# Optimization experiments

Hardware: AMD Instinct MI355X
Metric: run time of the kernel (lower is better)

Reference implementation:

```python
import jax, jax.numpy as jnp
import numpy as np

B, N, NB, P = 4, 2048, 10, 5
BIG = 1.0e5  # fill value for non-positive gt grasps


def _build_grasps(approach, base, contacts, thickness):
    # approach/base/contacts: [B,N,3], thickness: [B,N] -> [B,N,4,4]
    cross = jnp.cross(approach, base)
    R = jnp.stack([base, cross, approach], axis=-1)            # columns: [base, cross, approach]
    t = contacts + thickness[..., None] * 0.5 * base           # [B,N,3]
    top = jnp.concatenate([R, t[..., None]], axis=-1)          # [B,N,3,4]
    bottom = jnp.broadcast_to(jnp.array([0.0, 0.0, 0.0, 1.0], top.dtype),
                              top.shape[:-2] + (1, 4))
    return jnp.concatenate([top, bottom], axis=-2)             # [B,N,4,4]


def _transform_cps(cp_h, grasps):
    # cp_h: [P,4], grasps: [B,N,4,4] -> transformed control points [B,N,P,3]
    # torch: matmul(control_points, grasps^T)[..., :3]
    return jnp.einsum('pk,bnjk->bnpj', cp_h, grasps)[..., :3]


def _pairwise_sq(a, b):
    # a: [B,Na,P,3], b: [B,Nb,P,3] -> [B,Na,Nb] = sum_{p,c} (a-b)^2
    af = a.reshape(a.shape[0], a.shape[1], -1)
    bf = b.reshape(b.shape[0], b.shape[1], -1)
    a2 = jnp.sum(af * af, axis=-1)
    b2 = jnp.sum(bf * bf, axis=-1)
    d = a2[:, :, None] + b2[:, None, :] - 2.0 * jnp.einsum('bnd,bmd->bnm', af, bf)
    return jnp.maximum(d, 0.0)


def _forward(grasp_dir_head, approach_dir_head, grasp_offset_head, pred_points,
             binary_score_pred, binary_score_head, dir_labels_pc_cam, offset_labels_pc,
             grasp_success_labels_pc, approach_labels_pc_cam, bin_vals, bin_weights,
             control_pts, sym_control_pts):
    succ = grasp_success_labels_pc                              # [B,N] in {0,1}
    pos_in_view = jnp.maximum(jnp.sum(succ, axis=1), 1.0)       # min_geom_loss_divisor = 1.0

    # bin_offsets=True: lookup bin value of argmax bin
    thickness_pred = bin_vals[jnp.argmax(grasp_offset_head, axis=2)]   # [B,N]
    thickness_gt = bin_vals[jnp.argmax(offset_labels_pc, axis=2)]      # [B,N]

    pred_grasps = _build_grasps(approach_dir_head, grasp_dir_head, pred_points, thickness_pred)
    gt_grasps = _build_grasps(approach_labels_pc_cam, dir_labels_pc_cam, pred_points, thickness_gt)
    mask4 = succ.astype(bool)[:, :, None, None]
    pos_gt_grasps = jnp.where(mask4, gt_grasps, jnp.full_like(gt_grasps, BIG))

    ones_col = jnp.ones((P, 1), dtype=control_pts.dtype)
    cp_h = jnp.concatenate([control_pts, ones_col], axis=1)      # [P,4]
    scp_h = jnp.concatenate([sym_control_pts, ones_col], axis=1)

    pred_cp = _transform_cps(cp_h, pred_grasps)                  # [B,N,P,3]
    gt_cp_pos = _transform_cps(cp_h, pos_gt_grasps)
    sym_gt_cp_pos = _transform_cps(scp_h, pos_gt_grasps)

    # pred -> gt ADD-S (top-k with k=1 == min over concat of the two [B,N,N])
    d1 = _pairwise_sq(pred_cp, gt_cp_pos)
    d2 = _pairwise_sq(pred_cp, sym_gt_cp_pos)
    best = jnp.min(jnp.minimum(d1, d2), axis=2)                  # [B,N]
    gate = jnp.minimum(jnp.sum(succ, axis=1, keepdims=True), 1.0)
    min_adds = gate * jnp.sqrt(best)
    adds_loss = jnp.mean(binary_score_pred[:, :, 0] * min_adds)

    # gt -> pred ADD-S with unmasked gt grasps + confidence gather
    gt_cp = _transform_cps(cp_h, gt_grasps)
    sym_gt_cp = _transform_cps(scp_h, gt_grasps)
    dg1 = _pairwise_sq(gt_cp, pred_cp)                           # [B,Ngt,Npred]
    dg2 = _pairwise_sq(sym_gt_cp, pred_cp)
    m1 = jnp.min(dg1, axis=2); i1 = jnp.argmin(dg1, axis=2)
    m2 = jnp.min(dg2, axis=2); i2 = jnp.argmin(dg2, axis=2)
    # torch: where(-m1 < -m2, sym_idcs, idcs) == pick sym when m2 < m1
    idcs = jnp.where(m2 < m1, i2, i1)                            # [B,N]
    min_g2p = jnp.minimum(m1, m2) * succ
    conf = jnp.take_along_axis(binary_score_pred[:, :, 0], idcs, axis=1)
    adds_loss_gt2pred = jnp.mean(jnp.sum(conf * min_g2p, axis=1) / pos_in_view)

    # direction cosine loss
    cos_d = 1.0 - jnp.sum(dir_labels_pc_cam * grasp_dir_head, axis=2)
    dir_cosine_loss = jnp.mean(jnp.sum(cos_d * succ, axis=1) / pos_in_view)

    # approach cosine loss against orthogonalized label
    proj = jnp.sum(grasp_dir_head * approach_labels_pc_cam, axis=2, keepdims=True)
    orthog = approach_labels_pc_cam - proj * grasp_dir_head
    orthog = orthog / jnp.maximum(jnp.linalg.norm(orthog, axis=2, keepdims=True), 1e-12)
    cos_a = 1.0 - jnp.sum(orthog * approach_dir_head, axis=2)
    approach_cosine_loss = jnp.mean(jnp.sum(cos_a * succ, axis=1) / pos_in_view)

    # per-bin sigmoid BCE offset loss, bin-weighted
    bce = (offset_labels_pc * jax.nn.softplus(-grasp_offset_head)
           + (1.0 - offset_labels_pc) * jax.nn.softplus(grasp_offset_head))
    off = jnp.mean(bin_weights[None, None, :] * bce, axis=2)
    offset_loss = jnp.mean(jnp.sum(off * succ, axis=1) / pos_in_view)

    # binary success score BCE
    s = succ[:, :, None]
    score_bce = (s * jax.nn.softplus(-binary_score_head)
                 + (1.0 - s) * jax.nn.softplus(binary_score_head))
    bin_ce_loss = jnp.mean(score_bce)

    total = (1.0 * dir_cosine_loss + 1.0 * bin_ce_loss + 1.0 * offset_loss
             + 1.0 * approach_cosine_loss + 10.0 * adds_loss + 1.0 * adds_loss_gt2pred)
    return total


def setup_inputs():
    key = jax.random.key(0)
    ks = jax.random.split(key, 14)
    unit = lambda x: x / jnp.linalg.norm(x, axis=-1, keepdims=True)
    grasp_dir_head = unit(jax.random.normal(ks[0], (B, N, 3), jnp.float32))
    approach_dir_head = unit(jax.random.normal(ks[1], (B, N, 3), jnp.float32))
    grasp_offset_head = jax.random.normal(ks[2], (B, N, NB), jnp.float32)
    pred_points = jax.random.normal(ks[3], (B, N, 3), jnp.float32) * 0.3
    binary_score_pred = jax.random.uniform(ks[4], (B, N, 1), jnp.float32)
    binary_score_head = jax.random.normal(ks[5], (B, N, 1), jnp.float32)
    dir_labels_pc_cam = unit(jax.random.normal(ks[6], (B, N, 3), jnp.float32))
    offset_labels_pc = jax.nn.one_hot(jax.random.randint(ks[7], (B, N), 0, NB), NB, dtype=jnp.float32)
    grasp_success_labels_pc = jnp.round(jax.random.uniform(ks[8], (B, N), jnp.float32))
    approach_labels_pc_cam = unit(jax.random.normal(ks[9], (B, N, 3), jnp.float32))
    bin_vals = jnp.sort(jax.random.uniform(ks[10], (NB,), jnp.float32) * 0.075)
    bin_weights = jax.random.uniform(ks[11], (NB,), jnp.float32) + 0.5
    control_pts = jax.random.normal(ks[12], (P, 3), jnp.float32) * 0.05
    sym_control_pts = control_pts[jnp.array([0, 1, 3, 2, 4])]  # finger-swapped (symmetric) gripper
    return {
        'grasp_dir_head': grasp_dir_head,
        'approach_dir_head': approach_dir_head,
        'grasp_offset_head': grasp_offset_head,
        'pred_points': pred_points,
        'binary_score_pred': binary_score_pred,
        'binary_score_head': binary_score_head,
        'dir_labels_pc_cam': dir_labels_pc_cam,
        'offset_labels_pc': offset_labels_pc,
        'grasp_success_labels_pc': grasp_success_labels_pc,
        'approach_labels_pc_cam': approach_labels_pc_cam,
        'bin_vals': bin_vals,
        'bin_weights': bin_weights,
        'control_pts': control_pts,
        'sym_control_pts': sym_control_pts,
    }


def reference(grasp_dir_head, approach_dir_head, grasp_offset_head, pred_points,
              binary_score_pred, binary_score_head, dir_labels_pc_cam, offset_labels_pc,
              grasp_success_labels_pc, approach_labels_pc_cam, bin_vals, bin_weights,
              control_pts, sym_control_pts):
    return _forward(grasp_dir_head, approach_dir_head, grasp_offset_head, pred_points,
                    binary_score_pred, binary_score_head, dir_labels_pc_cam, offset_labels_pc,
                    grasp_success_labels_pc, approach_labels_pc_cam, bin_vals, bin_weights,
                    control_pts, sym_control_pts)
```

## Files before the change

### kernel.cpp

```cpp
#include <hip/hip_runtime.h>

#define Bn 4
#define Nn 2048
#define NBn 10
#define BN (Bn*Nn)
#define TM 64

#define OFF_PRED 0
#define OFF_GT   (BN*16)
#define OFF_SYM  (2*BN*16)
#define OFF_PN2  (3*BN*16)
#define OFF_GN2  (OFF_PN2 + BN)
#define OFF_SN2  (OFF_GN2 + BN)
#define OFF_BEST (OFF_SN2 + BN)
#define OFF_PK1  (OFF_BEST + BN)
#define OFF_PK2  (OFF_PK1 + 2*BN)
#define OFF_PART (OFF_PK2 + 2*BN)

__device__ inline float sp_(float x) {
  return fmaxf(x, 0.0f) + log1pf(expf(-fabsf(x)));
}

__device__ inline float dot16_(const float4&a0,const float4&a1,const float4&a2,const float4&a3,
                               const float4&b0,const float4&b1,const float4&b2,const float4&b3){
  float s0 = fmaf(a0.w,b0.w, fmaf(a0.z,b0.z, fmaf(a0.y,b0.y, a0.x*b0.x)));
  float s1 = fmaf(a1.w,b1.w, fmaf(a1.z,b1.z, fmaf(a1.y,b1.y, a1.x*b1.x)));
  float s2 = fmaf(a2.w,b2.w, fmaf(a2.z,b2.z, fmaf(a2.y,b2.y, a2.x*b2.x)));
  float s3 = fmaf(a3.w,b3.w, fmaf(a3.z,b3.z, fmaf(a3.y,b3.y, a3.x*b3.x)));
  return (s0+s1)+(s2+s3);
}

__device__ inline float blockSum_(float v, float* red) {
  #pragma unroll
  for (int o = 32; o > 0; o >>= 1) v += __shfl_down(v, o, 64);
  __syncthreads();
  if ((threadIdx.x & 63) == 0) red[threadIdx.x >> 6] = v;
  __syncthreads();
  return red[0] + red[1] + red[2] + red[3];
}

__global__ __launch_bounds__(64) void k_prep(
    const float* __restrict__ gdir, const float* __restrict__ adirp,
    const float* __restrict__ goff, const float* __restrict__ ppts,
    const float* __restrict__ dlab, const float* __restrict__ olab,
    const float* __restrict__ alab,
    const float* __restrict__ binv,
    const float* __restrict__ cpts, const float* __restrict__ scpts,
    float* __restrict__ ws)
{
  const int idx = blockIdx.x * 64 + threadIdx.x;

  const float gd0=gdir[idx*3+0],  gd1=gdir[idx*3+1],  gd2=gdir[idx*3+2];
  const float ad0=adirp[idx*3+0], ad1=adirp[idx*3+1], ad2=adirp[idx*3+2];
  const float dl0=dlab[idx*3+0],  dl1=dlab[idx*3+1],  dl2=dlab[idx*3+2];
  const float al0=alab[idx*3+0],  al1=alab[idx*3+1],  al2=alab[idx*3+2];
  const float pt0=ppts[idx*3+0],  pt1=ppts[idx*3+1],  pt2=ppts[idx*3+2];

  float bv = goff[idx*NBn]; int ap = 0;
  #pragma unroll
  for (int k = 1; k < NBn; k++) { float v = goff[idx*NBn+k]; if (v > bv) { bv = v; ap = k; } }
  float bg = olab[idx*NBn]; int ag = 0;
  #pragma unroll
  for (int k = 1; k < NBn; k++) { float v = olab[idx*NBn+k]; if (v > bg) { bg = v; ag = k; } }
  const float tp = binv[ap] * 0.5f;
  const float tg = binv[ag] * 0.5f;

  const float cp0 = ad1*gd2 - ad2*gd1, cp1 = ad2*gd0 - ad0*gd2, cp2 = ad0*gd1 - ad1*gd0;
  const float cg0 = al1*dl2 - al2*dl1, cg1 = al2*dl0 - al0*dl2, cg2 = al0*dl1 - al1*dl0;
  const float tpx = pt0 + tp*gd0, tpy = pt1 + tp*gd1, tpz = pt2 + tp*gd2;
  const float tgx = pt0 + tg*dl0, tgy = pt1 + tg*dl1, tgz = pt2 + tg*dl2;

  float pcp[15], gcp[15], hcp[15];
  float pn2 = 0.f, gn2 = 0.f, sn2 = 0.f;
  #pragma unroll
  for (int p = 0; p < 5; p++) {
    const float cx = cpts[p*3], cy = cpts[p*3+1], cz = cpts[p*3+2];
    const float sx = scpts[p*3], sy = scpts[p*3+1], sz = scpts[p*3+2];
    float x, y, z;
    x = gd0*cx + cp0*cy + ad0*cz + tpx;
    y = gd1*cx + cp1*cy + ad1*cz + tpy;
    z = gd2*cx + cp2*cy + ad2*cz + tpz;
    pcp[p*3+0]=x; pcp[p*3+1]=y; pcp[p*3+2]=z;
    pn2 = fmaf(x,x, fmaf(y,y, fmaf(z,z, pn2)));
    x = dl0*cx + cg0*cy + al0*cz + tgx;
    y = dl1*cx + cg1*cy + al1*cz + tgy;
    z = dl2*cx + cg2*cy + al2*cz + tgz;
    gcp[p*3+0]=x; gcp[p*3+1]=y; gcp[p*3+2]=z;
    gn2 = fmaf(x,x, fmaf(y,y, fmaf(z,z, gn2)));
    x = dl0*sx + cg0*sy + al0*sz + tgx;
    y = dl1*sx + cg1*sy + al1*sz + tgy;
    z = dl2*sx + cg2*sy + al2*sz + tgz;
    hcp[p*3+0]=x; hcp[p*3+1]=y; hcp[p*3+2]=z;
    sn2 = fmaf(x,x, fmaf(y,y, fmaf(z,z, sn2)));
  }

  float4* pd = (float4*)(ws + OFF_PRED) + (size_t)idx*4;
  pd[0]=make_float4(pcp[0],pcp[1],pcp[2],pcp[3]);
  pd[1]=make_float4(pcp[4],pcp[5],pcp[6],pcp[7]);
  pd[2]=make_float4(pcp[8],pcp[9],pcp[10],pcp[11]);
  pd[3]=make_float4(pcp[12],pcp[13],pcp[14],0.f);
  float4* gdst = (float4*)(ws + OFF_GT) + (size_t)idx*4;
  gdst[0]=make_float4(gcp[0],gcp[1],gcp[2],gcp[3]);
  gdst[1]=make_float4(gcp[4],gcp[5],gcp[6],gcp[7]);
  gdst[2]=make_float4(gcp[8],gcp[9],gcp[10],gcp[11]);
  gdst[3]=make_float4(gcp[12],gcp[13],gcp[14],0.f);
  float4* sdst = (float4*)(ws + OFF_SYM) + (size_t)idx*4;
  sdst[0]=make_float4(hcp[0],hcp[1],hcp[2],hcp[3]);
  sdst[1]=make_float4(hcp[4],hcp[5],hcp[6],hcp[7]);
  sdst[2]=make_float4(hcp[8],hcp[9],hcp[10],hcp[11]);
  sdst[3]=make_float4(hcp[12],hcp[13],hcp[14],0.f);
  ws[OFF_PN2+idx] = pn2; ws[OFF_GN2+idx] = gn2; ws[OFF_SN2+idx] = sn2;

  ((unsigned*)ws)[OFF_BEST + idx] = 0x7F800000u;
  ((unsigned long long*)(ws + OFF_PK1))[idx] = ~0ull;
  ((unsigned long long*)(ws + OFF_PK2))[idx] = ~0ull;
}

__global__ __launch_bounds__(256) void k_pair(const float* __restrict__ succ,
                                              float* __restrict__ ws) {
  __shared__ float4 gts[TM][4], sys[TM][4], prs[TM][4];
  __shared__ float gb2[TM], sb2[TM], pb2[TM], msk[TM];
  const int mt = blockIdx.x, nt = blockIdx.y, b = blockIdx.z;
  const int tid = threadIdx.x;
  const int r = tid >> 2, p = tid & 3;
  const int mrow = b*Nn + mt*TM + r;
  gts[r][p] = ((const float4*)(ws + OFF_GT))  [(size_t)mrow*4 + p];
  sys[r][p] = ((const float4*)(ws + OFF_SYM)) [(size_t)mrow*4 + p];
  prs[r][p] = ((const float4*)(ws + OFF_PRED))[(size_t)mrow*4 + p];
  if      (p == 0) gb2[r] = ws[OFF_GN2 + mrow];
  else if (p == 1) sb2[r] = ws[OFF_SN2 + mrow];
  else if (p == 2) pb2[r] = ws[OFF_PN2 + mrow];
  else             msk[r] = succ[mrow];
  __syncthreads();

  const int nrow = b*Nn + nt*256 + tid;
  const float INF = __int_as_float(0x7F800000);

  {
    const float4* pa = (const float4*)(ws + OFF_PRED) + (size_t)nrow*4;
    const float4 a0 = pa[0], a1 = pa[1], a2 = pa[2], a3 = pa[3];
    const float an2 = ws[OFF_PN2 + nrow];
    float best = INF;
    for (int m = 0; m < TM; m++) {
      if (msk[m] != 0.0f) {
        const float d1 = fmaxf(fmaf(-2.f, dot16_(a0,a1,a2,a3, gts[m][0],gts[m][1],gts[m][2],gts[m][3]), an2 + gb2[m]), 0.f);
        const float d2 = fmaxf(fmaf(-2.f, dot16_(a0,a1,a2,a3, sys[m][0],sys[m][1],sys[m][2],sys[m][3]), an2 + sb2[m]), 0.f);
        best = fminf(best, fminf(d1, d2));
      }
    }
    if (best < INF)
      atomicMin((unsigned int*)ws + OFF_BEST + nrow, __float_as_uint(best));
  }

  {
    const float4* g = (const float4*)(ws + OFF_GT)  + (size_t)nrow*4;
    const float4 g0=g[0], g1=g[1], g2=g[2], g3=g[3];
    const float4* s = (const float4*)(ws + OFF_SYM) + (size_t)nrow*4;
    const float4 s0=s[0], s1=s[1], s2=s[2], s3=s[3];
    const float gn2 = ws[OFF_GN2 + nrow], sn2 = ws[OFF_SN2 + nrow];
    unsigned long long b1 = ~0ull, b2 = ~0ull;
    for (int m = 0; m < TM; m++) {
      const float4 p0 = prs[m][0], p1 = prs[m][1], p2 = prs[m][2], p3 = prs[m][3];
      const float pb = pb2[m];
      const float d1 = fmaxf(fmaf(-2.f, dot16_(g0,g1,g2,g3,p0,p1,p2,p3), gn2 + pb), 0.f);
      const float d2 = fmaxf(fmaf(-2.f, dot16_(s0,s1,s2,s3,p0,p1,p2,p3), sn2 + pb), 0.f);
      const unsigned long long c1 = ((unsigned long long)__float_as_uint(d1) << 32) | (unsigned)(mt*TM + m);
      const unsigned long long c2 = ((unsigned long long)__float_as_uint(d2) << 32) | (unsigned)(mt*TM + m);
      b1 = (c1 < b1) ? c1 : b1;
      b2 = (c2 < b2) ? c2 : b2;
    }
    atomicMin((unsigned long long*)(ws + OFF_PK1) + nrow, b1);
    atomicMin((unsigned long long*)(ws + OFF_PK2) + nrow, b2);
  }
}

__global__ __launch_bounds__(256) void k_red(
    const float* __restrict__ bsp,  const float* __restrict__ bsh,
    const float* __restrict__ succ,
    const float* __restrict__ gdir, const float* __restrict__ adirp,
    const float* __restrict__ dlab, const float* __restrict__ alab,
    const float* __restrict__ goff, const float* __restrict__ olab,
    const float* __restrict__ binw,
    float* __restrict__ ws)
{
  __shared__ float red[4];
  const int b = blockIdx.y, nt = blockIdx.x;
  const int idx = b*Nn + nt*256 + threadIdx.x;
  const float sc = succ[idx];

  const float best = __uint_as_float(((const unsigned*)ws)[OFF_BEST + idx]);
  const float adds = (best < 1e30f) ? bsp[idx] * sqrtf(best) : 0.f;

  const unsigned long long p1 = ((const unsigned long long*)(ws + OFF_PK1))[idx];
  const unsigned long long p2 = ((const unsigned long long*)(ws + OFF_PK2))[idx];
  const float m1 = __uint_as_float((unsigned)(p1 >> 32));
  const float m2 = __uint_as_float((unsigned)(p2 >> 32));
  const int   i1 = (int)(p1 & 0xffffffffull);
  const int   i2 = (int)(p2 & 0xffffffffull);
  const int   id = (m2 < m1) ? i2 : i1;
  const float g2p = bsp[b*Nn + id] * fminf(m1, m2) * sc;

  const float gd0=gdir[idx*3+0],  gd1=gdir[idx*3+1],  gd2=gdir[idx*3+2];
  const float ad0=adirp[idx*3+0], ad1=adirp[idx*3+1], ad2=adirp[idx*3+2];
  const float dl0=dlab[idx*3+0],  dl1=dlab[idx*3+1],  dl2=dlab[idx*3+2];
  const float al0=alab[idx*3+0],  al1=alab[idx*3+1],  al2=alab[idx*3+2];

  const float cosd = 1.f - (dl0*gd0 + dl1*gd1 + dl2*gd2);
  const float proj = gd0*al0 + gd1*al1 + gd2*al2;
  const float o0 = al0 - proj*gd0, o1 = al1 - proj*gd1, o2 = al2 - proj*gd2;
  const float on = sqrtf(o0*o0 + o1*o1 + o2*o2);
  const float inv = 1.f / fmaxf(on, 1e-12f);
  const float cosa = 1.f - inv*(o0*ad0 + o1*ad1 + o2*ad2);

  float offv = 0.f;
  #pragma unroll
  for (int k = 0; k < NBn; k++) {
    const float x = goff[idx*NBn+k], lab = olab[idx*NBn+k];
    const float bce = lab * sp_(-x) + (1.f - lab) * sp_(x);
    offv = fmaf(binw[k], bce, offv);
  }
  offv *= (1.0f / NBn);
  const float sb = bsh[idx];
  const float sbce = sc * sp_(-sb) + (1.f - sc) * sp_(sb);

  float* part = ws + OFF_PART + (size_t)(b*8 + nt)*8;
  float t;
  t = blockSum_(cosd*sc, red); if (threadIdx.x == 0) part[0] = t;
  t = blockSum_(cosa*sc, red); if (threadIdx.x == 0) part[1] = t;
  t = blockSum_(offv*sc, red); if (threadIdx.x == 0) part[2] = t;
  t = blockSum_(sc, red);      if (threadIdx.x == 0) part[3] = t;
  t = blockSum_(sbce, red);    if (threadIdx.x == 0) part[4] = t;
  t = blockSum_(adds, red);    if (threadIdx.x == 0) part[5] = t;
  t = blockSum_(g2p, red);     if (threadIdx.x == 0) part[6] = t;
}

__global__ __launch_bounds__(64) void k_fin(const float* __restrict__ ws, float* __restrict__ out) {
  const int t = threadIdx.x;
  float v[7];
  #pragma unroll
  for (int c = 0; c < 7; c++) v[c] = (t < 32) ? ws[OFF_PART + t*8 + c] : 0.f;
  #pragma unroll
  for (int o = 1; o < 8; o <<= 1) {
    #pragma unroll
    for (int c = 0; c < 7; c++) v[c] += __shfl_xor(v[c], o, 64);
  }
  const float pos = fmaxf(v[3], 1.f);
  float vb   = (v[0] + v[1] + v[2] + v[6]) / pos;
  float bce  = v[4];
  float adds = v[5];
  #pragma unroll
  for (int o = 8; o < 32; o <<= 1) {
    vb   += __shfl_xor(vb,   o, 64);
    bce  += __shfl_xor(bce,  o, 64);
    adds += __shfl_xor(adds, o, 64);
  }
  if (t == 0)
    out[0] = vb * 0.25f + bce * (1.f/BN) + 10.f * adds * (1.f/BN);
}

extern "C" void kernel_launch(void* const* d_in, const int* in_sizes, int n_in,
                              void* d_out, int out_size, void* d_ws, size_t ws_size,
                              hipStream_t stream) {
  const float* gdir  = (const float*)d_in[0];
  const float* adirp = (const float*)d_in[1];
  const float* goff  = (const float*)d_in[2];
  const float* ppts  = (const float*)d_in[3];
  const float* bsp   = (const float*)d_in[4];
  const float* bsh   = (const float*)d_in[5];
  const float* dlab  = (const float*)d_in[6];
  const float* olab  = (const float*)d_in[7];
  const float* succ  = (const float*)d_in[8];
  const float* alab  = (const float*)d_in[9];
  const float* binv  = (const float*)d_in[10];
  const float* binw  = (const float*)d_in[11];
  const float* cpts  = (const float*)d_in[12];
  const float* scpts = (const float*)d_in[13];
  float* ws  = (float*)d_ws;
  float* out = (float*)d_out;

  k_prep<<<dim3(BN/64), dim3(64), 0, stream>>>(gdir, adirp, goff, ppts,
                                               dlab, olab, alab, binv, cpts, scpts, ws);
  k_pair<<<dim3(Nn/TM, Nn/256, Bn), dim3(256), 0, stream>>>(succ, ws);
  k_red<<<dim3(Nn/256, Bn), dim3(256), 0, stream>>>(bsp, bsh, succ, gdir, adirp,
                                                    dlab, alab, goff, olab, binw, ws);
  k_fin<<<1, 64, 0, stream>>>(ws, out);
}
```

Before: 136.4 us.

## Fuse per-point losses into prep, register-block pair kernel, merge tail reductions

Moves the per-point direction, approach, offset and score BCE losses into the prep kernel, so one fewer kernel launch is needed and the inputs are read once. The pairwise kernel now gives each thread two query rows with a smaller M tile, replaces the success-mask branch with a large additive bias, and tracks the argmin in plain float/int before packing a single combined 64-bit atomic. The separate reduce and final kernels become one 1024-thread tail kernel. In exchange, the pair kernel uses more registers, the tail runs on a single block, and it relies on __threadfence_block rather than a barrier between the LDS writes and reads by other lanes.

```diff
diff --git a/kernel.cpp b/kernel.cpp
--- a/kernel.cpp
+++ b/kernel.cpp
@@ -4,7 +4,8 @@
 #define Nn 2048
 #define NBn 10
 #define BN (Bn*Nn)
-#define TM 64
+#define TM 32
+#define BIGM 1e32f
 
 #define OFF_PRED 0
 #define OFF_GT   (BN*16)
@@ -13,9 +14,8 @@
 #define OFF_GN2  (OFF_PN2 + BN)
 #define OFF_SN2  (OFF_GN2 + BN)
 #define OFF_BEST (OFF_SN2 + BN)
-#define OFF_PK1  (OFF_BEST + BN)
-#define OFF_PK2  (OFF_PK1 + 2*BN)
-#define OFF_PART (OFF_PK2 + 2*BN)
+#define OFF_PK   (OFF_BEST + BN)
+#define OFF_PART (OFF_PK + 2*BN)
 
 __device__ inline float sp_(float x) {
   return fmaxf(x, 0.0f) + log1pf(expf(-fabsf(x)));
@@ -39,22 +39,26 @@
   return red[0] + red[1] + red[2] + red[3];
 }
 
-__global__ __launch_bounds__(64) void k_prep(
+__global__ __launch_bounds__(256) void k_prep(
     const float* __restrict__ gdir, const float* __restrict__ adirp,
     const float* __restrict__ goff, const float* __restrict__ ppts,
+    const float* __restrict__ bsh,
     const float* __restrict__ dlab, const float* __restrict__ olab,
-    const float* __restrict__ alab,
-    const float* __restrict__ binv,
+    const float* __restrict__ succ, const float* __restrict__ alab,
+    const float* __restrict__ binv, const float* __restrict__ binw,
     const float* __restrict__ cpts, const float* __restrict__ scpts,
     float* __restrict__ ws)
 {
-  const int idx = blockIdx.x * 64 + threadIdx.x;
+  __shared__ float red[4];
+  const int pb = blockIdx.x;
+  const int idx = pb * 256 + threadIdx.x;
 
   const float gd0=gdir[idx*3+0],  gd1=gdir[idx*3+1],  gd2=gdir[idx*3+2];
   const float ad0=adirp[idx*3+0], ad1=adirp[idx*3+1], ad2=adirp[idx*3+2];
   const float dl0=dlab[idx*3+0],  dl1=dlab[idx*3+1],  dl2=dlab[idx*3+2];
   const float al0=alab[idx*3+0],  al1=alab[idx*3+1],  al2=alab[idx*3+2];
   const float pt0=ppts[idx*3+0],  pt1=ppts[idx*3+1],  pt2=ppts[idx*3+2];
+  const float sc = succ[idx];
 
   float bv = goff[idx*NBn]; int ap = 0;
   #pragma unroll
@@ -112,98 +116,7 @@
   ws[OFF_PN2+idx] = pn2; ws[OFF_GN2+idx] = gn2; ws[OFF_SN2+idx] = sn2;
 
   ((unsigned*)ws)[OFF_BEST + idx] = 0x7F800000u;
-  ((unsigned long long*)(ws + OFF_PK1))[idx] = ~0ull;
-  ((unsigned long long*)(ws + OFF_PK2))[idx] = ~0ull;
-}
-
-__global__ __launch_bounds__(256) void k_pair(const float* __restrict__ succ,
-                                              float* __restrict__ ws) {
-  __shared__ float4 gts[TM][4], sys[TM][4], prs[TM][4];
-  __shared__ float gb2[TM], sb2[TM], pb2[TM], msk[TM];
-  const int mt = blockIdx.x, nt = blockIdx.y, b = blockIdx.z;
-  const int tid = threadIdx.x;
-  const int r = tid >> 2, p = tid & 3;
-  const int mrow = b*Nn + mt*TM + r;
-  gts[r][p] = ((const float4*)(ws + OFF_GT))  [(size_t)mrow*4 + p];
-  sys[r][p] = ((const float4*)(ws + OFF_SYM)) [(size_t)mrow*4 + p];
-  prs[r][p] = ((const float4*)(ws + OFF_PRED))[(size_t)mrow*4 + p];
-  if      (p == 0) gb2[r] = ws[OFF_GN2 + mrow];
-  else if (p == 1) sb2[r] = ws[OFF_SN2 + mrow];
-  else if (p == 2) pb2[r] = ws[OFF_PN2 + mrow];
-  else             msk[r] = succ[mrow];
-  __syncthreads();
-
-  const int nrow = b*Nn + nt*256 + tid;
-  const float INF = __int_as_float(0x7F800000);
-
-  {
-    const float4* pa = (const float4*)(ws + OFF_PRED) + (size_t)nrow*4;
-    const float4 a0 = pa[0], a1 = pa[1], a2 = pa[2], a3 = pa[3];
-    const float an2 = ws[OFF_PN2 + nrow];
-    float best = INF;
-    for (int m = 0; m < TM; m++) {
-      if (msk[m] != 0.0f) {
-        const float d1 = fmaxf(fmaf(-2.f, dot16_(a0,a1,a2,a3, gts[m][0],gts[m][1],gts[m][2],gts[m][3]), an2 + gb2[m]), 0.f);
-        const float d2 = fmaxf(fmaf(-2.f, dot16_(a0,a1,a2,a3, sys[m][0],sys[m][1],sys[m][2],sys[m][3]), an2 + sb2[m]), 0.f);
-        best = fminf(best, fminf(d1, d2));
-      }
-    }
-    if (best < INF)
-      atomicMin((unsigned int*)ws + OFF_BEST + nrow, __float_as_uint(best));
-  }
-
-  {
-    const float4* g = (const float4*)(ws + OFF_GT)  + (size_t)nrow*4;
-    const float4 g0=g[0], g1=g[1], g2=g[2], g3=g[3];
-    const float4* s = (const float4*)(ws + OFF_SYM) + (size_t)nrow*4;
-    const float4 s0=s[0], s1=s[1], s2=s[2], s3=s[3];
-    const float gn2 = ws[OFF_GN2 + nrow], sn2 = ws[OFF_SN2 + nrow];
-    unsigned long long b1 = ~0ull, b2 = ~0ull;
-    for (int m = 0; m < TM; m++) {
-      const float4 p0 = prs[m][0], p1 = prs[m][1], p2 = prs[m][2], p3 = prs[m][3];
-      const float pb = pb2[m];
-      const float d1 = fmaxf(fmaf(-2.f, dot16_(g0,g1,g2,g3,p0,p1,p2,p3), gn2 + pb), 0.f);
-      const float d2 = fmaxf(fmaf(-2.f, dot16_(s0,s1,s2,s3,p0,p1,p2,p3), sn2 + pb), 0.f);
-      const unsigned long long c1 = ((unsigned long long)__float_as_uint(d1) << 32) | (unsigned)(mt*TM + m);
-      const unsigned long long c2 = ((unsigned long long)__float_as_uint(d2) << 32) | (unsigned)(mt*TM + m);
-      b1 = (c1 < b1) ? c1 : b1;
-      b2 = (c2 < b2) ? c2 : b2;
-    }
-    atomicMin((unsigned long long*)(ws + OFF_PK1) + nrow, b1);
-    atomicMin((unsigned long long*)(ws + OFF_PK2) + nrow, b2);
-  }
-}
-
-__global__ __launch_bounds__(256) void k_red(
-    const float* __restrict__ bsp,  const float* __restrict__ bsh,
-    const float* __restrict__ succ,
-    const float* __restrict__ gdir, const float* __restrict__ adirp,
-    const float* __restrict__ dlab, const float* __restrict__ alab,
-    const float* __restrict__ goff, const float* __restrict__ olab,
-    const float* __restrict__ binw,
-    float* __restrict__ ws)
-{
-  __shared__ float red[4];
-  const int b = blockIdx.y, nt = blockIdx.x;
-  const int idx = b*Nn + nt*256 + threadIdx.x;
-  const float sc = succ[idx];
-
-  const float best = __uint_as_float(((const unsigned*)ws)[OFF_BEST + idx]);
-  const float adds = (best < 1e30f) ? bsp[idx] * sqrtf(best) : 0.f;
-
-  const unsigned long long p1 = ((const unsigned long long*)(ws + OFF_PK1))[idx];
-  const unsigned long long p2 = ((const unsigned long long*)(ws + OFF_PK2))[idx];
-  const float m1 = __uint_as_float((unsigned)(p1 >> 32));
-  const float m2 = __uint_as_float((unsigned)(p2 >> 32));
-  const int   i1 = (int)(p1 & 0xffffffffull);
-  const int   i2 = (int)(p2 & 0xffffffffull);
-  const int   id = (m2 < m1) ? i2 : i1;
-  const float g2p = bsp[b*Nn + id] * fminf(m1, m2) * sc;
-
-  const float gd0=gdir[idx*3+0],  gd1=gdir[idx*3+1],  gd2=gdir[idx*3+2];
-  const float ad0=adirp[idx*3+0], ad1=adirp[idx*3+1], ad2=adirp[idx*3+2];
-  const float dl0=dlab[idx*3+0],  dl1=dlab[idx*3+1],  dl2=dlab[idx*3+2];
-  const float al0=alab[idx*3+0],  al1=alab[idx*3+1],  al2=alab[idx*3+2];
+  ((unsigned long long*)(ws + OFF_PK))[idx] = ~0ull;
 
   const float cosd = 1.f - (dl0*gd0 + dl1*gd1 + dl2*gd2);
   const float proj = gd0*al0 + gd1*al1 + gd2*al2;
@@ -223,39 +136,160 @@
   const float sb = bsh[idx];
   const float sbce = sc * sp_(-sb) + (1.f - sc) * sp_(sb);
 
-  float* part = ws + OFF_PART + (size_t)(b*8 + nt)*8;
+  float* part = ws + OFF_PART + (size_t)pb*8;
   float t;
   t = blockSum_(cosd*sc, red); if (threadIdx.x == 0) part[0] = t;
   t = blockSum_(cosa*sc, red); if (threadIdx.x == 0) part[1] = t;
   t = blockSum_(offv*sc, red); if (threadIdx.x == 0) part[2] = t;
   t = blockSum_(sc, red);      if (threadIdx.x == 0) part[3] = t;
   t = blockSum_(sbce, red);    if (threadIdx.x == 0) part[4] = t;
-  t = blockSum_(adds, red);    if (threadIdx.x == 0) part[5] = t;
-  t = blockSum_(g2p, red);     if (threadIdx.x == 0) part[6] = t;
-}
-
-__global__ __launch_bounds__(64) void k_fin(const float* __restrict__ ws, float* __restrict__ out) {
+}
+
+__global__ __launch_bounds__(256, 4) void k_pair(const float* __restrict__ succ,
+                                                 float* __restrict__ ws) {
+  __shared__ float gts[TM*16], sys[TM*16], prs[TM*16];
+  __shared__ float gb2[TM], sb2[TM], pb2[TM];
+  const int mt = blockIdx.x, nt = blockIdx.y, b = blockIdx.z;
+  const int tid = threadIdx.x;
+  const int mbase = mt*TM;
+  {
+    const float2* gsrc = (const float2*)(ws + OFF_GT  + (size_t)(b*Nn + mbase)*16);
+    const float2* ssrc = (const float2*)(ws + OFF_SYM + (size_t)(b*Nn + mbase)*16);
+    const float2* psrc = (const float2*)(ws + OFF_PRED+ (size_t)(b*Nn + mbase)*16);
+    ((float2*)gts)[tid] = gsrc[tid];
+    ((float2*)sys)[tid] = ssrc[tid];
+    ((float2*)prs)[tid] = psrc[tid];
+    if (tid < TM) {
+      const int mrow = b*Nn + mbase + tid;
+      const float bias = (succ[mrow] != 0.f) ? 0.f : BIGM;
+      gb2[tid] = ws[OFF_GN2 + mrow] + bias;
+      sb2[tid] = ws[OFF_SN2 + mrow] + bias;
+      pb2[tid] = ws[OFF_PN2 + mrow];
+    }
+  }
+  __syncthreads();
+
+  const int nrow0 = b*Nn + nt*512 + tid;
+  const int nrow1 = nrow0 + 256;
+
+  {
+    const float4* pa0 = (const float4*)(ws + OFF_PRED) + (size_t)nrow0*4;
+    const float4 a00=pa0[0], a01=pa0[1], a02=pa0[2], a03=pa0[3];
+    const float4* pa1 = (const float4*)(ws + OFF_PRED) + (size_t)nrow1*4;
+    const float4 a10=pa1[0], a11=pa1[1], a12=pa1[2], a13=pa1[3];
+    const float an20 = ws[OFF_PN2+nrow0], an21 = ws[OFF_PN2+nrow1];
+    float best0 = 1e38f, best1 = 1e38f;
+    const float4* G = (const float4*)gts;
+    const float4* S = (const float4*)sys;
+    for (int m = 0; m < TM; m++) {
+      const float4 g0=G[m*4+0], g1=G[m*4+1], g2=G[m*4+2], g3=G[m*4+3];
+      const float4 s0=S[m*4+0], s1=S[m*4+1], s2=S[m*4+2], s3=S[m*4+3];
+      const float gb = gb2[m], sb = sb2[m];
+      float d;
+      d = fmaxf(fmaf(-2.f, dot16_(a00,a01,a02,a03,g0,g1,g2,g3), an20+gb), 0.f);
+      best0 = fminf(best0, d);
+      d = fmaxf(fmaf(-2.f, dot16_(a00,a01,a02,a03,s0,s1,s2,s3), an20+sb), 0.f);
+      best0 = fminf(best0, d);
+      d = fmaxf(fmaf(-2.f, dot16_(a10,a11,a12,a13,g0,g1,g2,g3), an21+gb), 0.f);
+      best1 = fminf(best1, d);
+      d = fmaxf(fmaf(-2.f, dot16_(a10,a11,a12,a13,s0,s1,s2,s3), an21+sb), 0.f);
+      best1 = fminf(best1, d);
+    }
+    atomicMin((unsigned*)ws + OFF_BEST + nrow0, __float_as_uint(best0));
+    atomicMin((unsigned*)ws + OFF_BEST + nrow1, __float_as_uint(best1));
+  }
+
+  {
+    const float4* gp0 = (const float4*)(ws + OFF_GT)  + (size_t)nrow0*4;
+    const float4 g00=gp0[0], g01=gp0[1], g02=gp0[2], g03=gp0[3];
+    const float4* sp0 = (const float4*)(ws + OFF_SYM) + (size_t)nrow0*4;
+    const float4 s00=sp0[0], s01=sp0[1], s02=sp0[2], s03=sp0[3];
+    const float4* gp1 = (const float4*)(ws + OFF_GT)  + (size_t)nrow1*4;
+    const float4 g10=gp1[0], g11=gp1[1], g12=gp1[2], g13=gp1[3];
+    const float4* sp1 = (const float4*)(ws + OFF_SYM) + (size_t)nrow1*4;
+    const float4 s10=sp1[0], s11=sp1[1], s12=sp1[2], s13=sp1[3];
+    const float gn20 = ws[OFF_GN2+nrow0], sn20 = ws[OFF_SN2+nrow0];
+    const float gn21 = ws[OFF_GN2+nrow1], sn21 = ws[OFF_SN2+nrow1];
+
+    float bd10=1e38f, bd20=1e38f, bd11=1e38f, bd21=1e38f;
+    int   bi10=0,     bi20=0,     bi11=0,     bi21=0;
+    const float4* P = (const float4*)prs;
+    for (int m = 0; m < TM; m++) {
+      const float4 p0=P[m*4+0], p1=P[m*4+1], p2=P[m*4+2], p3=P[m*4+3];
+      const float pb = pb2[m];
+      float d;
+      d = fmaxf(fmaf(-2.f, dot16_(g00,g01,g02,g03,p0,p1,p2,p3), gn20+pb), 0.f);
+      if (d < bd10) { bd10 = d; bi10 = m; }
+      d = fmaxf(fmaf(-2.f, dot16_(s00,s01,s02,s03,p0,p1,p2,p3), sn20+pb), 0.f);
+      if (d < bd20) { bd20 = d; bi20 = m; }
+      d = fmaxf(fmaf(-2.f, dot16_(g10,g11,g12,g13,p0,p1,p2,p3), gn21+pb), 0.f);
+      if (d < bd11) { bd11 = d; bi11 = m; }
+      d = fmaxf(fmaf(-2.f, dot16_(s10,s11,s12,s13,p0,p1,p2,p3), sn21+pb), 0.f);
+      if (d < bd21) { bd21 = d; bi21 = m; }
+    }
+    unsigned long long c1, c2, q;
+    c1 = ((unsigned long long)__float_as_uint(bd10) << 32) | (unsigned)(mbase + bi10);
+    c2 = ((unsigned long long)__float_as_uint(bd20) << 32) | (unsigned)(2048 + mbase + bi20);
+    q = (c1 < c2) ? c1 : c2;
+    atomicMin((unsigned long long*)(ws + OFF_PK) + nrow0, q);
+    c1 = ((unsigned long long)__float_as_uint(bd11) << 32) | (unsigned)(mbase + bi11);
+    c2 = ((unsigned long long)__float_as_uint(bd21) << 32) | (unsigned)(2048 + mbase + bi21);
+    q = (c1 < c2) ? c1 : c2;
+    atomicMin((unsigned long long*)(ws + OFF_PK) + nrow1, q);
+  }
+}
+
+__global__ __launch_bounds__(1024) void k_tail(const float* __restrict__ bsp,
+                                               const float* __restrict__ succ,
+                                               const float* __restrict__ ws,
+                                               float* __restrict__ out) {
+  __shared__ float wadds[16], wg2p[16];
+  __shared__ float ldsA[4], ldsP[4], ldsG[4];
   const int t = threadIdx.x;
-  float v[7];
-  #pragma unroll
-  for (int c = 0; c < 7; c++) v[c] = (t < 32) ? ws[OFF_PART + t*8 + c] : 0.f;
+  const int b = t >> 8;
+  float adds = 0.f, g2p = 0.f;
+  #pragma unroll
+  for (int i = 0; i < 8; i++) {
+    const int idx = t*8 + i;
+    const float best = __uint_as_float(((const unsigned*)ws)[OFF_BEST + idx]);
+    if (best < 1e30f) adds += bsp[idx] * sqrtf(best);
+    const unsigned long long q = ((const unsigned long long*)(ws + OFF_PK))[idx];
+    const float d = __uint_as_float((unsigned)(q >> 32));
+    const int  id = (int)(q & 2047ull);
+    g2p += bsp[b*Nn + id] * d * succ[idx];
+  }
+  #pragma unroll
+  for (int o = 32; o > 0; o >>= 1) { adds += __shfl_down(adds, o, 64); g2p += __shfl_down(g2p, o, 64); }
+  if ((t & 63) == 0) { wadds[t>>6] = adds; wg2p[t>>6] = g2p; }
+  __syncthreads();
+  if (t >= 64) return;
+
+  float v0=0.f, v1=0.f, v2=0.f, v3=0.f, v4=0.f;
+  if (t < 32) {
+    const float* part = ws + OFF_PART + (size_t)t*8;
+    v0=part[0]; v1=part[1]; v2=part[2]; v3=part[3]; v4=part[4];
+  }
   #pragma unroll
   for (int o = 1; o < 8; o <<= 1) {
-    #pragma unroll
-    for (int c = 0; c < 7; c++) v[c] += __shfl_xor(v[c], o, 64);
-  }
-  const float pos = fmaxf(v[3], 1.f);
-  float vb   = (v[0] + v[1] + v[2] + v[6]) / pos;
-  float bce  = v[4];
-  float adds = v[5];
-  #pragma unroll
-  for (int o = 8; o < 32; o <<= 1) {
-    vb   += __shfl_xor(vb,   o, 64);
-    bce  += __shfl_xor(bce,  o, 64);
-    adds += __shfl_xor(adds, o, 64);
-  }
+    v0 += __shfl_xor(v0,o,64); v1 += __shfl_xor(v1,o,64);
+    v2 += __shfl_xor(v2,o,64); v3 += __shfl_xor(v3,o,64);
+    v4 += __shfl_xor(v4,o,64);
+  }
+  float bce = v4;
+  bce += __shfl_xor(bce,8,64); bce += __shfl_xor(bce,16,64);
+  float ga = (t<16) ? wg2p[t] : 0.f;
+  ga += __shfl_xor(ga,1,64); ga += __shfl_xor(ga,2,64);
+  float aa = (t<16) ? wadds[t] : 0.f;
+  aa += __shfl_xor(aa,1,64); aa += __shfl_xor(aa,2,64);
+  aa += __shfl_xor(aa,4,64); aa += __shfl_xor(aa,8,64);
+  if (t<32 && (t&7)==0) { ldsA[t>>3] = v0+v1+v2; ldsP[t>>3] = v3; }
+  if (t<16 && (t&3)==0) { ldsG[t>>2] = ga; }
+  __threadfence_block();
+  float vb = 0.f;
+  if (t < 4) vb = (ldsA[t] + ldsG[t]) / fmaxf(ldsP[t], 1.f);
+  vb += __shfl_xor(vb,1,64); vb += __shfl_xor(vb,2,64);
   if (t == 0)
-    out[0] = vb * 0.25f + bce * (1.f/BN) + 10.f * adds * (1.f/BN);
+    out[0] = vb * 0.25f + bce * (1.f/BN) + 10.f * aa * (1.f/BN);
 }
 
 extern "C" void kernel_launch(void* const* d_in, const int* in_sizes, int n_in,
@@ -278,10 +312,9 @@
   float* ws  = (float*)d_ws;
   float* out = (float*)d_out;
 
-  k_prep<<<dim3(BN/64), dim3(64), 0, stream>>>(gdir, adirp, goff, ppts,
-                                               dlab, olab, alab, binv, cpts, scpts, ws);
-  k_pair<<<dim3(Nn/TM, Nn/256, Bn), dim3(256), 0, stream>>>(succ, ws);
-  k_red<<<dim3(Nn/256, Bn), dim3(256), 0, stream>>>(bsp, bsh, succ, gdir, adirp,
-                                                    dlab, alab, goff, olab, binw, ws);
-  k_fin<<<1, 64, 0, stream>>>(ws, out);
-}
+  k_prep<<<dim3(BN/256), dim3(256), 0, stream>>>(gdir, adirp, goff, ppts, bsh,
+                                                 dlab, olab, succ, alab,
+                                                 binv, binw, cpts, scpts, ws);
+  k_pair<<<dim3(Nn/TM, Nn/512, Bn), dim3(256), 0, stream>>>(succ, ws);
+  k_tail<<<1, 1024, 0, stream>>>(bsp, succ, ws, out);
+}
```

Result: slower. 149.7 us (+9.7%).
